# Kernel optimization log

Hardware: AMD Instinct MI355X
Metric: run time of the kernel (lower is better)

## Reference

```python
import jax, jax.numpy as jnp
import numpy as np

B, S, N_CLASS = 16, 2048, 8
T0, T1 = 0.0, 100.0
EPS = 1e-8


def setup_inputs() -> dict:
    key = jax.random.key(0)
    k1, k2, k3, k4, k5 = jax.random.split(key, 5)
    # event times sorted along the sequence dim (Hawkes history is causal)
    ts = jnp.sort(jax.random.uniform(k1, (B, S), minval=0.0, maxval=T1, dtype=jnp.float32), axis=1)
    ms = jax.random.randint(k2, (B, S), 0, N_CLASS, dtype=jnp.int32)
    mu = jax.random.uniform(k3, (N_CLASS,), minval=0.05, maxval=0.2, dtype=jnp.float32)
    alphas = jax.random.uniform(k4, (N_CLASS, N_CLASS), minval=0.01, maxval=0.1, dtype=jnp.float32)
    beta = jax.random.uniform(k5, (N_CLASS,), minval=0.5, maxval=2.0, dtype=jnp.float32)
    return {"ts": ts, "ms": ms, "mu": mu, "alphas": alphas, "beta": beta}


def reference(ts, ms, mu, alphas, beta):
    # ts: [B,S] float times; ms: [B,S] int event types
    valid = ts > 0                                          # [B,S]
    # causal pair mask j < i, combined with event validity of both endpoints
    tri = jnp.tril(jnp.ones((S, S), dtype=bool), k=-1)      # [S,S]
    pair_valid = tri[None, :, :] & valid[:, :, None] & valid[:, None, :]
    # time differences t_i - t_j, zeroed where masked (avoids exp overflow)
    tds = jnp.where(pair_valid, ts[:, :, None] - ts[:, None, :], 0.0)
    a_ij = alphas[ms[:, :, None], ms[:, None, :]]           # [B,S,S] alpha[m_i, m_j]
    b_j = beta[ms][:, None, :]                              # [B,1,S] beta[m_j]
    K = a_ij * b_j * jnp.exp(-b_j * tds) * pair_valid       # [B,S,S]
    lams = K.sum(-1) + mu[ms]                               # [B,S]
    sumlog = (jnp.log(lams + EPS) * valid).sum()
    baserate = mu.sum() * (T1 - T0)
    # compensator integral: sum_i alpha[:,m_i].sum() * (1 - exp(-beta[m_i]*(T1 - t_i)))
    temp_int = 1.0 - jnp.exp(-beta[ms] * (T1 - ts))         # [B,S]
    alpha_int = alphas[:, ms].sum(0)                        # [B,S]
    integ = (alpha_int * temp_int * valid).sum()
    return sumlog - baserate - integ
```

## Files before the change

kernel.cpp:

```cpp
#include <hip/hip_runtime.h>
#include <math.h>

#define BB 16
#define SS 2048
#define NC 8
#define TILE 256
#define NT (SS/TILE)
#define TRI (NT*(NT+1)/2)
#define LOG2E 1.4426950408889634f
#define T1V 100.0f
#define EPSV 1e-8f

__device__ __forceinline__ float fexp2(float x) {
#if __has_builtin(__builtin_amdgcn_exp2f)
    return __builtin_amdgcn_exp2f(x);
#else
    return exp2f(x);
#endif
}

__global__ __launch_bounds__(TILE) void hawkes_pairs(
    const float* __restrict__ ts, const int* __restrict__ ms,
    const float* __restrict__ alphas, const float* __restrict__ beta,
    float* __restrict__ lam_ws)
{
    __shared__ float sh_u[TILE];
    __shared__ float sh_p[TILE];
    __shared__ int   sh_m[TILE];
    __shared__ float sh_ab[NC*NC];

    int blk = blockIdx.x;
    int b = blk / TRI;
    int r = blk % TRI;
    int it = 0;
    while ((it+1)*(it+2)/2 <= r) ++it;
    int jc = r - it*(it+1)/2;

    int tid = threadIdx.x;
    if (tid < NC*NC) {
        int row = tid / NC, col = tid % NC;
        sh_ab[tid] = alphas[row*NC+col] * beta[col];
    }

    int jg = jc*TILE + tid;
    float tj = ts[b*SS + jg];
    int   mj = ms[b*SS + jg];
    float pj = beta[mj] * LOG2E;
    sh_u[tid] = (tj > 0.0f) ? pj * tj : -1e30f;
    sh_p[tid] = pj;
    sh_m[tid] = mj;
    __syncthreads();

    int ig = it*TILE + tid;
    float ti = ts[b*SS + ig];
    int   mi = ms[b*SS + ig];
    const float* abrow = &sh_ab[mi*NC];
    float acc = 0.0f;

    if (jc < it) {
        #pragma unroll 8
        for (int j = 0; j < TILE; ++j) {
            float arg = fmaf(-sh_p[j], ti, sh_u[j]);
            float e   = fexp2(arg);
            acc = fmaf(abrow[sh_m[j]], e, acc);
        }
    } else {
        #pragma unroll 4
        for (int j = 0; j < TILE; ++j) {
            float arg = fmaf(-sh_p[j], ti, sh_u[j]);
            float e   = fexp2(arg);
            float v   = (j < tid) ? abrow[sh_m[j]] * e : 0.0f;
            acc += v;
        }
    }
    atomicAdd(&lam_ws[b*SS + ig], acc);
}

__global__ __launch_bounds__(256) void hawkes_finalize(
    const float* __restrict__ ts, const int* __restrict__ ms,
    const float* __restrict__ mu, const float* __restrict__ alphas,
    const float* __restrict__ beta, const float* __restrict__ lam_ws,
    float* __restrict__ out)
{
    __shared__ float sh_acol[NC];
    int tid = threadIdx.x;
    if (tid < NC) {
        float s = 0.0f;
        for (int rr = 0; rr < NC; ++rr) s += alphas[rr*NC + tid];
        sh_acol[tid] = s;
    }
    __syncthreads();

    int idx = blockIdx.x * 256 + tid;
    float t = ts[idx];
    int   m = ms[idx];
    float contrib = 0.0f;
    if (t > 0.0f) {
        float lam = lam_ws[idx] + mu[m];
        contrib = logf(lam + EPSV);
        float tint = 1.0f - fexp2(-beta[m] * LOG2E * (T1V - t));
        contrib -= sh_acol[m] * tint;
    }

    for (int off = 32; off > 0; off >>= 1)
        contrib += __shfl_down(contrib, off, 64);
    __shared__ float wsum[4];
    int lane = tid & 63, w = tid >> 6;
    if (lane == 0) wsum[w] = contrib;
    __syncthreads();
    if (tid == 0) {
        float s = wsum[0] + wsum[1] + wsum[2] + wsum[3];
        atomicAdd(out, s);
    }
    if (idx == 0) {
        float msum = 0.0f;
        for (int c = 0; c < NC; ++c) msum += mu[c];
        atomicAdd(out, -msum * (T1V - 0.0f));
    }
}

extern "C" void kernel_launch(void* const* d_in, const int* in_sizes, int n_in,
                              void* d_out, int out_size, void* d_ws, size_t ws_size,
                              hipStream_t stream) {
    const float* ts     = (const float*)d_in[0];
    const int*   ms     = (const int*)d_in[1];
    const float* mu     = (const float*)d_in[2];
    const float* alphas = (const float*)d_in[3];
    const float* beta   = (const float*)d_in[4];
    float* out    = (float*)d_out;
    float* lam_ws = (float*)d_ws;

    hipMemsetAsync(lam_ws, 0, BB*SS*sizeof(float), stream);
    hipMemsetAsync(out, 0, sizeof(float), stream);

    hawkes_pairs<<<BB*TRI, TILE, 0, stream>>>(ts, ms, alphas, beta, lam_ws);
    hawkes_finalize<<<(BB*SS)/256, 256, 0, stream>>>(ts, ms, mu, alphas, beta, lam_ws, out);
}
```

Before: 94.44 us.

## Replace O(S^2) pair sum with per-class exponential-decay tile summaries

Exploits the separable exponential kernel: each 128-event tile is summarized by per-class decayed sums anchored at its last event, and later tiles combine these summaries with a single decay factor per class. Only within-tile pairs are computed directly, and the finalize step is fused into the main kernel. This removes the quadratic cross-tile pair work and the lambda workspace memset. In exchange it relies on sorted times and on exp2 of large positive arguments staying finite, which risks precision loss or overflow when time gaps are large.

```diff
diff --git a/kernel.cpp b/kernel.cpp
--- a/kernel.cpp
+++ b/kernel.cpp
@@ -4,10 +4,10 @@
 #define BB 16
 #define SS 2048
 #define NC 8
-#define TILE 256
+#define TILE 128
 #define NT (SS/TILE)
-#define TRI (NT*(NT+1)/2)
 #define LOG2E 1.4426950408889634f
+#define LN2   0.6931471805599453f
 #define T1V 100.0f
 #define EPSV 1e-8f
 
@@ -18,102 +18,135 @@
     return exp2f(x);
 #endif
 }
+__device__ __forceinline__ float flog2(float x) {
+#if __has_builtin(__builtin_amdgcn_logf)
+    return __builtin_amdgcn_logf(x);
+#else
+    return log2f(x);
+#endif
+}
 
-__global__ __launch_bounds__(TILE) void hawkes_pairs(
+__global__ __launch_bounds__(TILE) void hawkes_tilesum(
     const float* __restrict__ ts, const int* __restrict__ ms,
-    const float* __restrict__ alphas, const float* __restrict__ beta,
-    float* __restrict__ lam_ws)
+    const float* __restrict__ beta, float* __restrict__ E)
 {
-    __shared__ float sh_u[TILE];
+    int b = blockIdx.x / NT;
+    int T = blockIdx.x % NT;
+    int tid = threadIdx.x;
+    int jg = b*SS + T*TILE + tid;
+
+    float tj = ts[jg];
+    int   mj = ms[jg];
+    float tref = ts[b*SS + T*TILE + TILE-1];
+    float p  = beta[mj] * LOG2E;
+    float e  = (tj > 0.0f) ? fexp2(p * (tj - tref)) : 0.0f;
+
+    int lane = tid & 63, wave = tid >> 6;
+    __shared__ float shw[2*NC];
+    #pragma unroll
+    for (int c = 0; c < NC; ++c) {
+        float v = (mj == c) ? e : 0.0f;
+        for (int off = 32; off; off >>= 1) v += __shfl_xor(v, off, 64);
+        if (lane == 0) shw[wave*NC + c] = v;
+    }
+    __syncthreads();
+    if (tid < NC) E[(b*NT + T)*NC + tid] = shw[tid] + shw[NC + tid];
+}
+
+__global__ __launch_bounds__(TILE) void hawkes_main(
+    const float* __restrict__ ts, const int* __restrict__ ms,
+    const float* __restrict__ mu, const float* __restrict__ alphas,
+    const float* __restrict__ beta, const float* __restrict__ E,
+    float* __restrict__ out)
+{
+    int b = blockIdx.x / NT;
+    int T = blockIdx.x % NT;
+    int tid = threadIdx.x;
+
+    __shared__ float sh_ab[NC*NC];
+    __shared__ float sh_acol[NC];
+    __shared__ float sh_pc[NC];
+    __shared__ float sh_g[NC];
+    __shared__ float sh_pu[TILE];
     __shared__ float sh_p[TILE];
     __shared__ int   sh_m[TILE];
-    __shared__ float sh_ab[NC*NC];
 
-    int blk = blockIdx.x;
-    int b = blk / TRI;
-    int r = blk % TRI;
-    int it = 0;
-    while ((it+1)*(it+2)/2 <= r) ++it;
-    int jc = r - it*(it+1)/2;
-
-    int tid = threadIdx.x;
     if (tid < NC*NC) {
-        int row = tid / NC, col = tid % NC;
-        sh_ab[tid] = alphas[row*NC+col] * beta[col];
+        int col = tid & (NC-1);
+        sh_ab[tid] = alphas[tid] * beta[col];
+    }
+    if (tid < NC) {
+        float s = 0.0f;
+        #pragma unroll
+        for (int r = 0; r < NC; ++r) s += alphas[r*NC + tid];
+        sh_acol[tid] = s;
+        sh_pc[tid] = beta[tid] * LOG2E;
     }
 
-    int jg = jc*TILE + tid;
-    float tj = ts[b*SS + jg];
-    int   mj = ms[b*SS + jg];
-    float pj = beta[mj] * LOG2E;
-    sh_u[tid] = (tj > 0.0f) ? pj * tj : -1e30f;
-    sh_p[tid] = pj;
-    sh_m[tid] = mj;
+    int ig = b*SS + T*TILE + tid;
+    float ti = ts[ig];
+    int   mi = ms[ig];
+    float pi = beta[mi] * LOG2E;
+    sh_p[tid]  = pi;
+    sh_pu[tid] = (ti > 0.0f) ? pi * ti : -1e30f;
+    sh_m[tid]  = mi;
+
+    float anchor = (T > 0) ? ts[b*SS + T*TILE - 1] : 0.0f;
+    if (tid < NC) {
+        float g = 0.0f;
+        if (T > 0) {
+            float pc = beta[tid] * LOG2E;
+            for (int Tp = 0; Tp < T; ++Tp) {
+                float tr = ts[b*SS + Tp*TILE + TILE-1];
+                g += fexp2(pc * (tr - anchor)) * E[(b*NT + Tp)*NC + tid];
+            }
+        }
+        sh_g[tid] = g;
+    }
     __syncthreads();
 
-    int ig = it*TILE + tid;
-    float ti = ts[b*SS + ig];
-    int   mi = ms[b*SS + ig];
     const float* abrow = &sh_ab[mi*NC];
     float acc = 0.0f;
 
-    if (jc < it) {
-        #pragma unroll 8
-        for (int j = 0; j < TILE; ++j) {
-            float arg = fmaf(-sh_p[j], ti, sh_u[j]);
-            float e   = fexp2(arg);
-            acc = fmaf(abrow[sh_m[j]], e, acc);
-        }
-    } else {
-        #pragma unroll 4
-        for (int j = 0; j < TILE; ++j) {
-            float arg = fmaf(-sh_p[j], ti, sh_u[j]);
-            float e   = fexp2(arg);
-            float v   = (j < tid) ? abrow[sh_m[j]] * e : 0.0f;
-            acc += v;
+    if (T > 0) {
+        #pragma unroll
+        for (int c = 0; c < NC; ++c) {
+            float dec = fexp2(sh_pc[c] * (anchor - ti));
+            acc = fmaf(abrow[c] * sh_g[c], dec, acc);
         }
     }
-    atomicAdd(&lam_ws[b*SS + ig], acc);
-}
 
-__global__ __launch_bounds__(256) void hawkes_finalize(
-    const float* __restrict__ ts, const int* __restrict__ ms,
-    const float* __restrict__ mu, const float* __restrict__ alphas,
-    const float* __restrict__ beta, const float* __restrict__ lam_ws,
-    float* __restrict__ out)
-{
-    __shared__ float sh_acol[NC];
-    int tid = threadIdx.x;
-    if (tid < NC) {
-        float s = 0.0f;
-        for (int rr = 0; rr < NC; ++rr) s += alphas[rr*NC + tid];
-        sh_acol[tid] = s;
+    int wave = tid >> 6, lane = tid & 63;
+    int jfull = wave * 64;
+    for (int j = 0; j < jfull; ++j) {
+        float arg = fmaf(-sh_p[j], ti, sh_pu[j]);
+        acc = fmaf(abrow[sh_m[j]], fexp2(arg), acc);
     }
-    __syncthreads();
-
-    int idx = blockIdx.x * 256 + tid;
-    float t = ts[idx];
-    int   m = ms[idx];
-    float contrib = 0.0f;
-    if (t > 0.0f) {
-        float lam = lam_ws[idx] + mu[m];
-        contrib = logf(lam + EPSV);
-        float tint = 1.0f - fexp2(-beta[m] * LOG2E * (T1V - t));
-        contrib -= sh_acol[m] * tint;
+    #pragma unroll 4
+    for (int jj = 0; jj < 64; ++jj) {
+        int j = jfull + jj;
+        float arg = fmaf(-sh_p[j], ti, sh_pu[j]);
+        float v = (jj < lane) ? abrow[sh_m[j]] * fexp2(arg) : 0.0f;
+        acc += v;
     }
 
-    for (int off = 32; off > 0; off >>= 1)
-        contrib += __shfl_down(contrib, off, 64);
-    __shared__ float wsum[4];
-    int lane = tid & 63, w = tid >> 6;
-    if (lane == 0) wsum[w] = contrib;
+    float contrib = 0.0f;
+    if (ti > 0.0f) {
+        float lam = acc + mu[mi];
+        contrib = flog2(lam + EPSV) * LN2;
+        float tint = 1.0f - fexp2(-pi * (T1V - ti));
+        contrib -= sh_acol[mi] * tint;
+    }
+
+    for (int off = 32; off; off >>= 1) contrib += __shfl_xor(contrib, off, 64);
+    __shared__ float shred[2];
+    if (lane == 0) shred[wave] = contrib;
     __syncthreads();
-    if (tid == 0) {
-        float s = wsum[0] + wsum[1] + wsum[2] + wsum[3];
-        atomicAdd(out, s);
-    }
-    if (idx == 0) {
+    if (tid == 0) atomicAdd(out, shred[0] + shred[1]);
+
+    if (blockIdx.x == 0 && tid == 0) {
         float msum = 0.0f;
+        #pragma unroll
         for (int c = 0; c < NC; ++c) msum += mu[c];
         atomicAdd(out, -msum * (T1V - 0.0f));
     }
@@ -127,12 +160,10 @@
     const float* mu     = (const float*)d_in[2];
     const float* alphas = (const float*)d_in[3];
     const float* beta   = (const float*)d_in[4];
-    float* out    = (float*)d_out;
-    float* lam_ws = (float*)d_ws;
+    float* out = (float*)d_out;
+    float* E   = (float*)d_ws;
 
-    hipMemsetAsync(lam_ws, 0, BB*SS*sizeof(float), stream);
     hipMemsetAsync(out, 0, sizeof(float), stream);
-
-    hawkes_pairs<<<BB*TRI, TILE, 0, stream>>>(ts, ms, alphas, beta, lam_ws);
-    hawkes_finalize<<<(BB*SS)/256, 256, 0, stream>>>(ts, ms, mu, alphas, beta, lam_ws, out);
+    hawkes_tilesum<<<BB*NT, TILE, 0, stream>>>(ts, ms, beta, E);
+    hawkes_main<<<BB*NT, TILE, 0, stream>>>(ts, ms, mu, alphas, beta, E, out);
 }
```

After: 76.33 us. 19.2% less time.
